# Kernel tuning notes

Measured on AMD Instinct MI355X. Metric: run time of the kernel, lower is better.

The kernel has to match this reference:

```python
import jax, jax.numpy as jnp
import numpy as np

D_MODEL = 1024
NUM_HEADS = 16
SEQ_LEN = 2048
BATCH = 2
THETA = 10000.0


def apply_rope(x, positions, theta=THETA):
    # x: [b, h, s, d]; positions: [s] int
    d = x.shape[-1]
    inv_freq = 1.0 / (theta ** (jnp.arange(0, d, 2, dtype=jnp.float32) / d))  # [d/2]
    ang = positions.astype(jnp.float32)[:, None] * inv_freq[None, :]  # [s, d/2]
    cos, sin = jnp.cos(ang), jnp.sin(ang)  # [s, d/2]
    x_even = x[..., 0::2]
    x_odd = x[..., 1::2]
    out_even = x_even * cos - x_odd * sin
    out_odd = x_even * sin + x_odd * cos
    # re-interleave pairs
    out = jnp.stack([out_even, out_odd], axis=-1).reshape(x.shape)
    return out


def setup_inputs() -> dict:
    key = jax.random.key(0)
    ks = jax.random.split(key, 5)
    scale = 1.0 / np.sqrt(D_MODEL)
    return {
        "in_features": jax.random.normal(ks[0], (BATCH, SEQ_LEN, D_MODEL), dtype=jnp.float32),
        "token_positions": jnp.arange(SEQ_LEN, dtype=jnp.int32),
        "q_w": jax.random.normal(ks[1], (D_MODEL, D_MODEL), dtype=jnp.float32) * scale,
        "k_w": jax.random.normal(ks[2], (D_MODEL, D_MODEL), dtype=jnp.float32) * scale,
        "v_w": jax.random.normal(ks[3], (D_MODEL, D_MODEL), dtype=jnp.float32) * scale,
        "o_w": jax.random.normal(ks[4], (D_MODEL, D_MODEL), dtype=jnp.float32) * scale,
    }


def reference(in_features, token_positions, q_w, k_w, v_w, o_w):
    b, s, _ = in_features.shape
    h = NUM_HEADS
    d_k = D_MODEL // h

    # Linear stores weights [out, in]: y = x @ W^T
    def proj(x, w):
        y = jnp.einsum('bsi,oi->bso', x, w)
        return y.reshape(b, s, h, d_k).transpose(0, 2, 1, 3)  # [b, h, s, d]

    q = apply_rope(proj(in_features, q_w), token_positions)
    k = apply_rope(proj(in_features, k_w), token_positions)
    v = proj(in_features, v_w)

    scores = jnp.einsum('bhqd,bhkd->bhqk', q, k) / jnp.sqrt(jnp.float32(d_k))
    causal = jnp.tril(jnp.ones((s, s), dtype=bool))
    scores = jnp.where(causal, scores, jnp.float32(-1e30))
    attn = jax.nn.softmax(scores, axis=-1)
    out = jnp.einsum('bhqk,bhkd->bhqd', attn, v)  # [b, h, s, d]
    out = out.transpose(0, 2, 1, 3).reshape(b, s, h * d_k)
    return jnp.einsum('bsi,oi->bso', out, o_w)
```

## Files before the change

### kernel.cpp

```cpp
#include <hip/hip_runtime.h>
#include <hip/hip_bf16.h>

typedef unsigned short ushort_t;
typedef unsigned int uint_t;
typedef __attribute__((ext_vector_type(4))) float f32x4;
typedef __attribute__((ext_vector_type(16))) float f32x16;
typedef __attribute__((ext_vector_type(8))) short short8;
typedef __attribute__((ext_vector_type(4))) short short4x;
typedef __attribute__((ext_vector_type(4))) unsigned short u16x4;
typedef __attribute__((ext_vector_type(2))) uint_t u32x2;

typedef const __attribute__((address_space(1))) unsigned char glob_t;
typedef __attribute__((address_space(3))) unsigned char lds_t;

#define S_LEN 2048
#define DM 1024
#define NH 16
#define DH 64
#define NB 2
#define BH (NB*NH)
#define MROWS (NB*S_LEN)

#define SCALE_L2E 0.18033688f

__device__ __forceinline__ float bf2f(ushort_t u) {
    return __uint_as_float(((uint_t)u) << 16);
}
__device__ __forceinline__ ushort_t f2bf(float f) {
    __hip_bfloat16 h = __float2bfloat16(f);
    return *reinterpret_cast<ushort_t*>(&h);
}

__global__ __launch_bounds__(256) void convert_all(
    const float* __restrict__ X,  const float* __restrict__ Wq,
    const float* __restrict__ Wk, const float* __restrict__ Wv,
    const float* __restrict__ Wo,
    ushort_t* __restrict__ Xb,  ushort_t* __restrict__ Wqb,
    ushort_t* __restrict__ Wkb, ushort_t* __restrict__ Wvb,
    ushort_t* __restrict__ Wob)
{
    size_t i = (size_t)blockIdx.x * 256 + threadIdx.x;
    size_t e = i * 4;
    const float* src; ushort_t* dst; size_t off;
    if (e < (size_t)MROWS * DM) { src = X; dst = Xb; off = e; }
    else {
        size_t r = e - (size_t)MROWS * DM;
        int w = (int)(r >> 20); off = r & 1048575;
        src = (w == 0) ? Wq : (w == 1) ? Wk : (w == 2) ? Wv : Wo;
        dst = (w == 0) ? Wqb : (w == 1) ? Wkb : (w == 2) ? Wvb : Wob;
    }
    float4 v = *reinterpret_cast<const float4*>(src + off);
    u16x4 o;
    o[0] = f2bf(v.x); o[1] = f2bf(v.y); o[2] = f2bf(v.z); o[3] = f2bf(v.w);
    *reinterpret_cast<u16x4*>(dst + off) = o;
}

__global__ __launch_bounds__(256) void rope_table_k(
    const int* __restrict__ pos, float2* __restrict__ tab)
{
    int i = blockIdx.x * 256 + threadIdx.x;
    int s = i >> 5, f = i & 31;
    float inv = powf(10000.0f, -(float)f / 32.0f);
    float ang = (float)pos[s] * inv;
    tab[i] = make_float2(cosf(ang), sinf(ang));
}

template<int MODE>
__global__ __launch_bounds__(256) void gemm128b(
    const ushort_t* __restrict__ A,
    const ushort_t* __restrict__ W0, const ushort_t* __restrict__ W1,
    const ushort_t* __restrict__ W2,
    ushort_t* __restrict__ D0, ushort_t* __restrict__ D1,
    ushort_t* __restrict__ D2,
    float* __restrict__ Fout, const float2* __restrict__ tab)
{
    __shared__ __attribute__((aligned(16))) ushort_t As[128 * 32];
    __shared__ __attribute__((aligned(16))) ushort_t Bs[128 * 32];
    const ushort_t* W = (MODE == 1 || blockIdx.z == 0) ? W0
                        : (blockIdx.z == 1 ? W1 : W2);
    ushort_t* Dst = (blockIdx.z == 0) ? D0 : (blockIdx.z == 1) ? D1 : D2;
    int m0 = blockIdx.x * 128, n0 = blockIdx.y * 128;
    int tid = threadIdx.x, lane = tid & 63, wv = tid >> 6;
    int wm = wv >> 1, wn = wv & 1;
    int l15 = lane & 15, g = lane >> 4;

    f32x4 acc[4][4];
    for (int i = 0; i < 4; i++)
        for (int j = 0; j < 4; j++)
            acc[i][j] = (f32x4){0.f, 0.f, 0.f, 0.f};

    int srow = wv * 32 + (lane >> 2);
    int scol = (lane & 3) * 8;
    const ushort_t* Ap = A + (size_t)(m0 + srow) * DM + scol;
    const ushort_t* Wp = W + (size_t)(n0 + srow) * DM + scol;
    lds_t* laA0 = (lds_t*)&As[wv * 1024];
    lds_t* laA1 = (lds_t*)&As[wv * 1024 + 512];
    lds_t* laB0 = (lds_t*)&Bs[wv * 1024];
    lds_t* laB1 = (lds_t*)&Bs[wv * 1024 + 512];

    for (int kk = 0; kk < DM; kk += 32) {
        __builtin_amdgcn_global_load_lds((glob_t*)(Ap + kk), laA0, 16, 0, 0);
        __builtin_amdgcn_global_load_lds((glob_t*)(Ap + 16 * DM + kk), laA1, 16, 0, 0);
        __builtin_amdgcn_global_load_lds((glob_t*)(Wp + kk), laB0, 16, 0, 0);
        __builtin_amdgcn_global_load_lds((glob_t*)(Wp + 16 * DM + kk), laB1, 16, 0, 0);
        __syncthreads();
        short8 af[4], bf[4];
        for (int i = 0; i < 4; i++)
            af[i] = *reinterpret_cast<const short8*>(
                &As[(wm * 64 + i * 16 + l15) * 32 + g * 8]);
        for (int j = 0; j < 4; j++)
            bf[j] = *reinterpret_cast<const short8*>(
                &Bs[(wn * 64 + j * 16 + l15) * 32 + g * 8]);
        __builtin_amdgcn_s_setprio(1);
        for (int i = 0; i < 4; i++)
            for (int j = 0; j < 4; j++)
                acc[i][j] = __builtin_amdgcn_mfma_f32_16x16x32_bf16(
                    af[i], bf[j], acc[i][j], 0, 0, 0);
        __builtin_amdgcn_s_setprio(0);
        __syncthreads();
    }

    for (int i = 0; i < 4; i++) {
        for (int j = 0; j < 4; j++) {
            int mbase = m0 + wm * 64 + i * 16 + g * 4;
            int n = n0 + wn * 64 + j * 16 + l15;
            if (MODE == 0) {
                int h = n >> 6, d = n & 63;
                if (blockIdx.z < 2) {
                    int f = d >> 1;
                    float sgn = (d & 1) ? 1.f : -1.f;
                    float sc = (blockIdx.z == 0) ? SCALE_L2E : 1.0f;
                    for (int r = 0; r < 4; r++) {
                        int m = mbase + r;
                        int b = m >> 11, s = m & 2047;
                        float v = acc[i][j][r];
                        float p = __shfl_xor(v, 1);
                        float2 cs = tab[s * 32 + f];
                        float out = (v * cs.x + p * cs.y * sgn) * sc;
                        Dst[(((size_t)(b * NH + h)) * S_LEN + s) * DH + d] =
                            f2bf(out);
                    }
                } else {
                    for (int r = 0; r < 4; r++) {
                        int m = mbase + r;
                        int b = m >> 11, s = m & 2047;
                        Dst[((size_t)(b * NH + h) * DH + d) * S_LEN + s] =
                            f2bf(acc[i][j][r]);
                    }
                }
            } else {
                for (int r = 0; r < 4; r++)
                    Fout[(size_t)(mbase + r) * DM + n] = acc[i][j][r];
            }
        }
    }
}

#define WAITV4 asm volatile("s_waitcnt vmcnt(4)" ::: "memory")
#define WAITV0 asm volatile("s_waitcnt vmcnt(0)" ::: "memory")

__global__ __launch_bounds__(512, 1) void attn_k10(
    const ushort_t* __restrict__ Q, const ushort_t* __restrict__ K,
    const ushort_t* __restrict__ Vt, ushort_t* __restrict__ O)
{
    __shared__ __attribute__((aligned(16))) ushort_t Ks[3][8192];
    __shared__ __attribute__((aligned(16))) ushort_t Vs[3][8192];

    int tid = threadIdx.x, wv = tid >> 6, lane = tid & 63;
    int l31 = lane & 31, h = lane >> 5, r7 = l31 & 7;
    int bid = blockIdx.x;
    int p = bid >> 5;
    int bh = bid & 31;
    int uB = 15 - p;
    int myu = (wv < 4) ? uB : p;
    int qmin = myu * 128 + (wv & 3) * 32, qmax = qmin + 31;
    int ntr = uB + 1;

    const ushort_t* Qp = Q + (size_t)bh * S_LEN * DH;
    const char* Kp = (const char*)(K + (size_t)bh * S_LEN * DH);
    const char* Vp = (const char*)(Vt + (size_t)bh * DH * S_LEN);

    short8 qf[4];
    {
        const ushort_t* qp = Qp + (((size_t)(qmin + l31)) << 6) + h * 8;
        #pragma unroll
        for (int ds = 0; ds < 4; ds++)
            qf[ds] = *reinterpret_cast<const short8*>(qp + ds * 16);
    }

    f32x16 oacc[2];
    oacc[0] = (f32x16){0.f};
    oacc[1] = (f32x16){0.f};
    float m_run = -INFINITY, l_run = 0.f;

#define STAGE10(buf, kk0) do {                                                \
    _Pragma("unroll") for (int c_ = 0; c_ < 2; ++c_) {                        \
        int Lk_ = c_ * 8192 + tid * 16;                                       \
        int rk_ = Lk_ >> 7;                                                   \
        int ck_ = (Lk_ & 127) ^ ((rk_ & 7) << 4);                             \
        __builtin_amdgcn_global_load_lds(                                     \
            (glob_t*)(Kp + (size_t)((kk0) + rk_) * 128 + ck_),                \
            (lds_t*)((char*)&Ks[buf][0] + c_ * 8192 + wv * 1024), 16, 0, 0);  \
        int rv_ = Lk_ >> 8;                                                   \
        int cb_ = Lk_ & 255;                                                  \
        int cv_ = ((cb_ & 127) ^ ((rv_ & 7) << 4)) | (cb_ & 128);             \
        __builtin_amdgcn_global_load_lds(                                     \
            (glob_t*)(Vp + (size_t)rv_ * (S_LEN * 2) + (size_t)(kk0) * 2      \
                      + cv_),                                                 \
            (lds_t*)((char*)&Vs[buf][0] + c_ * 8192 + wv * 1024), 16, 0, 0);  \
    } } while (0)

    STAGE10(0, 0);
    STAGE10(1, 128);
    WAITV4;
    __builtin_amdgcn_s_barrier();

    int cs = 0;
    for (int t = 0; t < ntr; ++t) {
        int k0 = t << 7;
        int s2 = (cs >= 1) ? cs - 1 : cs + 2;
        bool willstage = (t + 2 < ntr);
        if (willstage) STAGE10(s2, (t + 2) << 7);

        if (k0 <= qmax) {
            const char* kb = (const char*)&Ks[cs][0];
            const char* vbp = (const char*)&Vs[cs][0];

            f32x16 st[4];
            #pragma unroll
            for (int s = 0; s < 4; s++) {
                short8 kf[4];
                #pragma unroll
                for (int ds = 0; ds < 4; ds++)
                    kf[ds] = *reinterpret_cast<const short8*>(
                        kb + (s * 32 + l31) * 128 + (((h + 2 * ds) ^ r7) << 4));
                __builtin_amdgcn_s_setprio(1);
                f32x16 z = {0.f};
                #pragma unroll
                for (int ds = 0; ds < 4; ds++)
                    z = __builtin_amdgcn_mfma_f32_32x32x16_bf16(
                        kf[ds], qf[ds], z, 0, 0, 0);
                st[s] = z;
                __builtin_amdgcn_s_setprio(0);
            }

            if (k0 + 127 > qmin) {
                int q = qmin + l31;
                #pragma unroll
                for (int s = 0; s < 4; s++)
                    #pragma unroll
                    for (int r = 0; r < 16; r++)
                        if ((k0 + s * 32 + (r & 3) + 8 * (r >> 2) + 4 * h) > q)
                            st[s][r] = -1e30f;
            }

            float mv[4];
            #pragma unroll
            for (int s = 0; s < 4; s++) {
                float a0 = fmaxf(st[s][0], st[s][1]);
                float a1 = fmaxf(st[s][2], st[s][3]);
                float a2 = fmaxf(st[s][4], st[s][5]);
                float a3 = fmaxf(st[s][6], st[s][7]);
                float a4 = fmaxf(st[s][8], st[s][9]);
                float a5 = fmaxf(st[s][10], st[s][11]);
                float a6 = fmaxf(st[s][12], st[s][13]);
                float a7 = fmaxf(st[s][14], st[s][15]);
                mv[s] = fmaxf(fmaxf(fmaxf(a0, a1), fmaxf(a2, a3)),
                              fmaxf(fmaxf(a4, a5), fmaxf(a6, a7)));
            }
            float m16 = fmaxf(fmaxf(mv[0], mv[1]), fmaxf(mv[2], mv[3]));
            m16 = fmaxf(m16, __shfl_xor(m16, 32));

            if (!__all(m16 <= m_run + 11.5f)) {
                float m_new = fmaxf(m_run, m16);
                float alpha = exp2f(m_run - m_new);
                m_run = m_new;
                l_run *= alpha;
                oacc[0] *= alpha;
                oacc[1] *= alpha;
            }

            float ps = 0.f;
            short4x pa[4][4];
            #pragma unroll
            for (int s = 0; s < 4; s++)
                #pragma unroll
                for (int kt = 0; kt < 4; kt++) {
                    float p0 = exp2f(st[s][4 * kt + 0] - m_run);
                    float p1 = exp2f(st[s][4 * kt + 1] - m_run);
                    float p2 = exp2f(st[s][4 * kt + 2] - m_run);
                    float p3 = exp2f(st[s][4 * kt + 3] - m_run);
                    ps += (p0 + p1) + (p2 + p3);
                    u32x2 w = { (uint_t)f2bf(p0) | ((uint_t)f2bf(p1) << 16),
                                (uint_t)f2bf(p2) | ((uint_t)f2bf(p3) << 16) };
                    pa[s][kt] = __builtin_bit_cast(short4x, w);
                }
            ps += __shfl_xor(ps, 32);
            l_run += ps;

            #pragma unroll
            for (int s = 0; s < 4; s++) {
                short4x vb[2][4];
                #pragma unroll
                for (int db = 0; db < 2; db++)
                    #pragma unroll
                    for (int kt = 0; kt < 4; kt++) {
                        int c = s * 4 + kt;
                        vb[db][kt] = *reinterpret_cast<const short4x*>(
                            vbp + (db * 32 + l31) * 256
                            + ((((c & 7) ^ r7) << 4) | ((c >> 3) << 7))
                            + h * 8);
                    }
                __builtin_amdgcn_s_setprio(1);
                #pragma unroll
                for (int kt = 0; kt < 4; kt++) {
                    oacc[0] = __builtin_amdgcn_mfma_f32_32x32x8bf16_1k(
                        vb[0][kt], pa[s][kt], oacc[0], 0, 0, 0);
                    oacc[1] = __builtin_amdgcn_mfma_f32_32x32x8bf16_1k(
                        vb[1][kt], pa[s][kt], oacc[1], 0, 0, 0);
                }
                __builtin_amdgcn_s_setprio(0);
            }
        }

        if (willstage) { WAITV4; } else { WAITV0; }
        __builtin_amdgcn_s_barrier();
        cs = (cs >= 2) ? 0 : cs + 1;
    }

    float inv = 1.0f / l_run;
    int b = bh >> 4, head = bh & 15;
    int q_row = qmin + l31;
    size_t obase = ((size_t)b * S_LEN + q_row) * DM + head * DH;
    #pragma unroll
    for (int db = 0; db < 2; db++)
        #pragma unroll
        for (int rg = 0; rg < 4; rg++) {
            u16x4 o;
            #pragma unroll
            for (int j = 0; j < 4; j++)
                o[j] = f2bf(oacc[db][rg * 4 + j] * inv);
            *reinterpret_cast<u16x4*>(&O[obase + db * 32 + rg * 8 + h * 4]) = o;
        }
#undef STAGE10
}

extern "C" void kernel_launch(void* const* d_in, const int* in_sizes, int n_in,
                              void* d_out, int out_size, void* d_ws, size_t ws_size,
                              hipStream_t stream)
{
    const float* X  = (const float*)d_in[0];
    const int* pos  = (const int*)d_in[1];
    const float* qw = (const float*)d_in[2];
    const float* kw = (const float*)d_in[3];
    const float* vw = (const float*)d_in[4];
    const float* ow = (const float*)d_in[5];
    float* out = (float*)d_out;

    char* ws = (char*)d_ws;
    ushort_t* Xb   = (ushort_t*)(ws);
    ushort_t* Wqb  = (ushort_t*)(ws + 8388608);
    ushort_t* Wkb  = (ushort_t*)(ws + 10485760);
    ushort_t* Wvb  = (ushort_t*)(ws + 12582912);
    ushort_t* Wob  = (ushort_t*)(ws + 14680064);
    ushort_t* Qbh  = (ushort_t*)(ws + 16777216);
    ushort_t* Kbh  = (ushort_t*)(ws + 25165824);
    ushort_t* Vtb  = (ushort_t*)(ws + 41943040);
    ushort_t* AttO = (ushort_t*)(ws + 50331648);
    float2*   tab  = (float2*)(ws + 58720256);

    convert_all<<<8192, 256, 0, stream>>>(X, qw, kw, vw, ow,
                                          Xb, Wqb, Wkb, Wvb, Wob);
    rope_table_k<<<256, 256, 0, stream>>>(pos, tab);
    gemm128b<0><<<dim3(32, 8, 3), 256, 0, stream>>>(
        Xb, Wqb, Wkb, Wvb, Qbh, Kbh, Vtb, nullptr, tab);
    attn_k10<<<256, 512, 0, stream>>>(Qbh, Kbh, Vtb, AttO);
    gemm128b<1><<<dim3(32, 8, 1), 256, 0, stream>>>(
        AttO, Wob, nullptr, nullptr, nullptr, nullptr, nullptr, out, tab);
}
```

Before: 132.5 us.

## Merge prep kernels and deepen GEMM K-tile to 64 with XOR-swizzled LDS

Merges the bf16 conversion kernel and the RoPE table kernel into one launch, saving one kernel launch. The projection GEMMs now stage a K-slab of 64 per iteration instead of 32, which halves the number of barrier pairs per tile. They also apply an XOR swizzle on the LDS column offset so that fragment reads avoid bank conflicts. LDS use rises to 32 KB per block, which could reduce occupancy.

```diff
diff --git a/kernel.cpp b/kernel.cpp
--- a/kernel.cpp
+++ b/kernel.cpp
@@ -31,42 +31,41 @@
     return *reinterpret_cast<ushort_t*>(&h);
 }
 
-__global__ __launch_bounds__(256) void convert_all(
+__global__ __launch_bounds__(256) void prep_all(
     const float* __restrict__ X,  const float* __restrict__ Wq,
     const float* __restrict__ Wk, const float* __restrict__ Wv,
-    const float* __restrict__ Wo,
+    const float* __restrict__ Wo, const int* __restrict__ pos,
     ushort_t* __restrict__ Xb,  ushort_t* __restrict__ Wqb,
     ushort_t* __restrict__ Wkb, ushort_t* __restrict__ Wvb,
-    ushort_t* __restrict__ Wob)
+    ushort_t* __restrict__ Wob, float2* __restrict__ tab)
 {
-    size_t i = (size_t)blockIdx.x * 256 + threadIdx.x;
-    size_t e = i * 4;
-    const float* src; ushort_t* dst; size_t off;
-    if (e < (size_t)MROWS * DM) { src = X; dst = Xb; off = e; }
-    else {
-        size_t r = e - (size_t)MROWS * DM;
-        int w = (int)(r >> 20); off = r & 1048575;
-        src = (w == 0) ? Wq : (w == 1) ? Wk : (w == 2) ? Wv : Wo;
-        dst = (w == 0) ? Wqb : (w == 1) ? Wkb : (w == 2) ? Wvb : Wob;
-    }
-    float4 v = *reinterpret_cast<const float4*>(src + off);
-    u16x4 o;
-    o[0] = f2bf(v.x); o[1] = f2bf(v.y); o[2] = f2bf(v.z); o[3] = f2bf(v.w);
-    *reinterpret_cast<u16x4*>(dst + off) = o;
-}
-
-__global__ __launch_bounds__(256) void rope_table_k(
-    const int* __restrict__ pos, float2* __restrict__ tab)
-{
-    int i = blockIdx.x * 256 + threadIdx.x;
-    int s = i >> 5, f = i & 31;
-    float inv = powf(10000.0f, -(float)f / 32.0f);
-    float ang = (float)pos[s] * inv;
-    tab[i] = make_float2(cosf(ang), sinf(ang));
+    int bid = blockIdx.x;
+    if (bid < 8192) {
+        size_t i = (size_t)bid * 256 + threadIdx.x;
+        size_t e = i * 4;
+        const float* src; ushort_t* dst; size_t off;
+        if (e < (size_t)MROWS * DM) { src = X; dst = Xb; off = e; }
+        else {
+            size_t r = e - (size_t)MROWS * DM;
+            int w = (int)(r >> 20); off = r & 1048575;
+            src = (w == 0) ? Wq : (w == 1) ? Wk : (w == 2) ? Wv : Wo;
+            dst = (w == 0) ? Wqb : (w == 1) ? Wkb : (w == 2) ? Wvb : Wob;
+        }
+        float4 v = *reinterpret_cast<const float4*>(src + off);
+        u16x4 o;
+        o[0] = f2bf(v.x); o[1] = f2bf(v.y); o[2] = f2bf(v.z); o[3] = f2bf(v.w);
+        *reinterpret_cast<u16x4*>(dst + off) = o;
+    } else {
+        int i = (bid - 8192) * 256 + threadIdx.x;
+        int s = i >> 5, f = i & 31;
+        float inv = powf(10000.0f, -(float)f / 32.0f);
+        float ang = (float)pos[s] * inv;
+        tab[i] = make_float2(cosf(ang), sinf(ang));
+    }
 }
 
 template<int MODE>
-__global__ __launch_bounds__(256) void gemm128b(
+__global__ __launch_bounds__(256) void gemm128c(
     const ushort_t* __restrict__ A,
     const ushort_t* __restrict__ W0, const ushort_t* __restrict__ W1,
     const ushort_t* __restrict__ W2,
@@ -74,8 +73,8 @@
     ushort_t* __restrict__ D2,
     float* __restrict__ Fout, const float2* __restrict__ tab)
 {
-    __shared__ __attribute__((aligned(16))) ushort_t As[128 * 32];
-    __shared__ __attribute__((aligned(16))) ushort_t Bs[128 * 32];
+    __shared__ __attribute__((aligned(16))) ushort_t As[128 * 64];
+    __shared__ __attribute__((aligned(16))) ushort_t Bs[128 * 64];
     const ushort_t* W = (MODE == 1 || blockIdx.z == 0) ? W0
                         : (blockIdx.z == 1 ? W1 : W2);
     ushort_t* Dst = (blockIdx.z == 0) ? D0 : (blockIdx.z == 1) ? D1 : D2;
@@ -83,40 +82,52 @@
     int tid = threadIdx.x, lane = tid & 63, wv = tid >> 6;
     int wm = wv >> 1, wn = wv & 1;
     int l15 = lane & 15, g = lane >> 4;
+    int r7s = (l15 & 7) << 4;
 
     f32x4 acc[4][4];
     for (int i = 0; i < 4; i++)
         for (int j = 0; j < 4; j++)
             acc[i][j] = (f32x4){0.f, 0.f, 0.f, 0.f};
 
-    int srow = wv * 32 + (lane >> 2);
-    int scol = (lane & 3) * 8;
-    const ushort_t* Ap = A + (size_t)(m0 + srow) * DM + scol;
-    const ushort_t* Wp = W + (size_t)(n0 + srow) * DM + scol;
-    lds_t* laA0 = (lds_t*)&As[wv * 1024];
-    lds_t* laA1 = (lds_t*)&As[wv * 1024 + 512];
-    lds_t* laB0 = (lds_t*)&Bs[wv * 1024];
-    lds_t* laB1 = (lds_t*)&Bs[wv * 1024 + 512];
-
-    for (int kk = 0; kk < DM; kk += 32) {
-        __builtin_amdgcn_global_load_lds((glob_t*)(Ap + kk), laA0, 16, 0, 0);
-        __builtin_amdgcn_global_load_lds((glob_t*)(Ap + 16 * DM + kk), laA1, 16, 0, 0);
-        __builtin_amdgcn_global_load_lds((glob_t*)(Wp + kk), laB0, 16, 0, 0);
-        __builtin_amdgcn_global_load_lds((glob_t*)(Wp + 16 * DM + kk), laB1, 16, 0, 0);
+    const char* Ab = (const char*)A;
+    const char* Wb = (const char*)W;
+
+    for (int kk = 0; kk < DM; kk += 64) {
+        #pragma unroll
+        for (int c = 0; c < 4; c++) {
+            int L = c * 4096 + tid * 16;
+            int row = L >> 7;
+            int colb = (L & 127) ^ ((row & 7) << 4);
+            __builtin_amdgcn_global_load_lds(
+                (glob_t*)(Ab + ((size_t)(m0 + row) * DM + kk) * 2 + colb),
+                (lds_t*)((char*)As + c * 4096 + wv * 1024), 16, 0, 0);
+            __builtin_amdgcn_global_load_lds(
+                (glob_t*)(Wb + ((size_t)(n0 + row) * DM + kk) * 2 + colb),
+                (lds_t*)((char*)Bs + c * 4096 + wv * 1024), 16, 0, 0);
+        }
         __syncthreads();
-        short8 af[4], bf[4];
-        for (int i = 0; i < 4; i++)
-            af[i] = *reinterpret_cast<const short8*>(
-                &As[(wm * 64 + i * 16 + l15) * 32 + g * 8]);
-        for (int j = 0; j < 4; j++)
-            bf[j] = *reinterpret_cast<const short8*>(
-                &Bs[(wn * 64 + j * 16 + l15) * 32 + g * 8]);
-        __builtin_amdgcn_s_setprio(1);
-        for (int i = 0; i < 4; i++)
+        #pragma unroll
+        for (int half = 0; half < 2; half++) {
+            short8 af[4], bf[4];
+            #pragma unroll
+            for (int i = 0; i < 4; i++)
+                af[i] = *reinterpret_cast<const short8*>(
+                    (const char*)As + (wm * 64 + i * 16 + l15) * 128
+                    + ((half * 64 + g * 16) ^ r7s));
+            #pragma unroll
             for (int j = 0; j < 4; j++)
-                acc[i][j] = __builtin_amdgcn_mfma_f32_16x16x32_bf16(
-                    af[i], bf[j], acc[i][j], 0, 0, 0);
-        __builtin_amdgcn_s_setprio(0);
+                bf[j] = *reinterpret_cast<const short8*>(
+                    (const char*)Bs + (wn * 64 + j * 16 + l15) * 128
+                    + ((half * 64 + g * 16) ^ r7s));
+            __builtin_amdgcn_s_setprio(1);
+            #pragma unroll
+            for (int i = 0; i < 4; i++)
+                #pragma unroll
+                for (int j = 0; j < 4; j++)
+                    acc[i][j] = __builtin_amdgcn_mfma_f32_16x16x32_bf16(
+                        af[i], bf[j], acc[i][j], 0, 0, 0);
+            __builtin_amdgcn_s_setprio(0);
+        }
         __syncthreads();
     }
 
@@ -369,12 +380,11 @@
     ushort_t* AttO = (ushort_t*)(ws + 50331648);
     float2*   tab  = (float2*)(ws + 58720256);
 
-    convert_all<<<8192, 256, 0, stream>>>(X, qw, kw, vw, ow,
-                                          Xb, Wqb, Wkb, Wvb, Wob);
-    rope_table_k<<<256, 256, 0, stream>>>(pos, tab);
-    gemm128b<0><<<dim3(32, 8, 3), 256, 0, stream>>>(
+    prep_all<<<8448, 256, 0, stream>>>(X, qw, kw, vw, ow, pos,
+                                       Xb, Wqb, Wkb, Wvb, Wob, tab);
+    gemm128c<0><<<dim3(32, 8, 3), 256, 0, stream>>>(
         Xb, Wqb, Wkb, Wvb, Qbh, Kbh, Vtb, nullptr, tab);
     attn_k10<<<256, 512, 0, stream>>>(Qbh, Kbh, Vtb, AttO);
-    gemm128b<1><<<dim3(32, 8, 1), 256, 0, stream>>>(
+    gemm128c<1><<<dim3(32, 8, 1), 256, 0, stream>>>(
         AttO, Wob, nullptr, nullptr, nullptr, nullptr, nullptr, out, tab);
 }
```

Result: slower. 137.0 us (+3.4%).

## Double-buffer attention K/V in 256-key chunks and merge prep kernels

Applied to the files above, without the earlier changes.

Attention now stages two 128-key tiles per iteration into a double buffer and waits with vmcnt(0) once per 256 keys. Previously it used a 3-deep ring with one barrier per 128 keys. This halves the barrier and loop overhead but reduces how far ahead loads run, and it increases LDS use. The bf16 conversion and RoPE table kernels are fused into one launch to save a kernel launch.

```diff
diff --git a/kernel.cpp b/kernel.cpp
--- a/kernel.cpp
+++ b/kernel.cpp
@@ -31,38 +31,37 @@
     return *reinterpret_cast<ushort_t*>(&h);
 }
 
-__global__ __launch_bounds__(256) void convert_all(
+__global__ __launch_bounds__(256) void prep_all(
     const float* __restrict__ X,  const float* __restrict__ Wq,
     const float* __restrict__ Wk, const float* __restrict__ Wv,
-    const float* __restrict__ Wo,
+    const float* __restrict__ Wo, const int* __restrict__ pos,
     ushort_t* __restrict__ Xb,  ushort_t* __restrict__ Wqb,
     ushort_t* __restrict__ Wkb, ushort_t* __restrict__ Wvb,
-    ushort_t* __restrict__ Wob)
+    ushort_t* __restrict__ Wob, float2* __restrict__ tab)
 {
-    size_t i = (size_t)blockIdx.x * 256 + threadIdx.x;
-    size_t e = i * 4;
-    const float* src; ushort_t* dst; size_t off;
-    if (e < (size_t)MROWS * DM) { src = X; dst = Xb; off = e; }
-    else {
-        size_t r = e - (size_t)MROWS * DM;
-        int w = (int)(r >> 20); off = r & 1048575;
-        src = (w == 0) ? Wq : (w == 1) ? Wk : (w == 2) ? Wv : Wo;
-        dst = (w == 0) ? Wqb : (w == 1) ? Wkb : (w == 2) ? Wvb : Wob;
-    }
-    float4 v = *reinterpret_cast<const float4*>(src + off);
-    u16x4 o;
-    o[0] = f2bf(v.x); o[1] = f2bf(v.y); o[2] = f2bf(v.z); o[3] = f2bf(v.w);
-    *reinterpret_cast<u16x4*>(dst + off) = o;
-}
-
-__global__ __launch_bounds__(256) void rope_table_k(
-    const int* __restrict__ pos, float2* __restrict__ tab)
-{
-    int i = blockIdx.x * 256 + threadIdx.x;
-    int s = i >> 5, f = i & 31;
-    float inv = powf(10000.0f, -(float)f / 32.0f);
-    float ang = (float)pos[s] * inv;
-    tab[i] = make_float2(cosf(ang), sinf(ang));
+    int bid = blockIdx.x;
+    if (bid < 8192) {
+        size_t i = (size_t)bid * 256 + threadIdx.x;
+        size_t e = i * 4;
+        const float* src; ushort_t* dst; size_t off;
+        if (e < (size_t)MROWS * DM) { src = X; dst = Xb; off = e; }
+        else {
+            size_t r = e - (size_t)MROWS * DM;
+            int w = (int)(r >> 20); off = r & 1048575;
+            src = (w == 0) ? Wq : (w == 1) ? Wk : (w == 2) ? Wv : Wo;
+            dst = (w == 0) ? Wqb : (w == 1) ? Wkb : (w == 2) ? Wvb : Wob;
+        }
+        float4 v = *reinterpret_cast<const float4*>(src + off);
+        u16x4 o;
+        o[0] = f2bf(v.x); o[1] = f2bf(v.y); o[2] = f2bf(v.z); o[3] = f2bf(v.w);
+        *reinterpret_cast<u16x4*>(dst + off) = o;
+    } else {
+        int i = (bid - 8192) * 256 + threadIdx.x;
+        int s = i >> 5, f = i & 31;
+        float inv = powf(10000.0f, -(float)f / 32.0f);
+        float ang = (float)pos[s] * inv;
+        tab[i] = make_float2(cosf(ang), sinf(ang));
+    }
 }
 
 template<int MODE>
@@ -156,15 +155,14 @@
     }
 }
 
-#define WAITV4 asm volatile("s_waitcnt vmcnt(4)" ::: "memory")
 #define WAITV0 asm volatile("s_waitcnt vmcnt(0)" ::: "memory")
 
-__global__ __launch_bounds__(512, 1) void attn_k10(
+__global__ __launch_bounds__(512, 1) void attn_k11(
     const ushort_t* __restrict__ Q, const ushort_t* __restrict__ K,
     const ushort_t* __restrict__ Vt, ushort_t* __restrict__ O)
 {
-    __shared__ __attribute__((aligned(16))) ushort_t Ks[3][8192];
-    __shared__ __attribute__((aligned(16))) ushort_t Vs[3][8192];
+    __shared__ __attribute__((aligned(16))) ushort_t Ks[2][2][8192];
+    __shared__ __attribute__((aligned(16))) ushort_t Vs[2][2][8192];
 
     int tid = threadIdx.x, wv = tid >> 6, lane = tid & 63;
     int l31 = lane & 31, h = lane >> 5, r7 = l31 & 7;
@@ -174,7 +172,7 @@
     int uB = 15 - p;
     int myu = (wv < 4) ? uB : p;
     int qmin = myu * 128 + (wv & 3) * 32, qmax = qmin + 31;
-    int ntr = uB + 1;
+    int ntr = (uB + 2) >> 1;
 
     const ushort_t* Qp = Q + (size_t)bh * S_LEN * DH;
     const char* Kp = (const char*)(K + (size_t)bh * S_LEN * DH);
@@ -193,139 +191,146 @@
     oacc[1] = (f32x16){0.f};
     float m_run = -INFINITY, l_run = 0.f;
 
-#define STAGE10(buf, kk0) do {                                                \
+#define STAGE13(buf, hf, kk0) do {                                            \
     _Pragma("unroll") for (int c_ = 0; c_ < 2; ++c_) {                        \
         int Lk_ = c_ * 8192 + tid * 16;                                       \
         int rk_ = Lk_ >> 7;                                                   \
         int ck_ = (Lk_ & 127) ^ ((rk_ & 7) << 4);                             \
         __builtin_amdgcn_global_load_lds(                                     \
             (glob_t*)(Kp + (size_t)((kk0) + rk_) * 128 + ck_),                \
-            (lds_t*)((char*)&Ks[buf][0] + c_ * 8192 + wv * 1024), 16, 0, 0);  \
+            (lds_t*)((char*)&Ks[buf][hf][0] + c_ * 8192 + wv * 1024),         \
+            16, 0, 0);                                                        \
         int rv_ = Lk_ >> 8;                                                   \
         int cb_ = Lk_ & 255;                                                  \
         int cv_ = ((cb_ & 127) ^ ((rv_ & 7) << 4)) | (cb_ & 128);             \
         __builtin_amdgcn_global_load_lds(                                     \
             (glob_t*)(Vp + (size_t)rv_ * (S_LEN * 2) + (size_t)(kk0) * 2      \
                       + cv_),                                                 \
-            (lds_t*)((char*)&Vs[buf][0] + c_ * 8192 + wv * 1024), 16, 0, 0);  \
+            (lds_t*)((char*)&Vs[buf][hf][0] + c_ * 8192 + wv * 1024),         \
+            16, 0, 0);                                                        \
     } } while (0)
 
-    STAGE10(0, 0);
-    STAGE10(1, 128);
-    WAITV4;
+    STAGE13(0, 0, 0);
+    STAGE13(0, 1, 128);
+    WAITV0;
     __builtin_amdgcn_s_barrier();
 
-    int cs = 0;
+    int buf = 0;
     for (int t = 0; t < ntr; ++t) {
-        int k0 = t << 7;
-        int s2 = (cs >= 1) ? cs - 1 : cs + 2;
-        bool willstage = (t + 2 < ntr);
-        if (willstage) STAGE10(s2, (t + 2) << 7);
-
-        if (k0 <= qmax) {
-            const char* kb = (const char*)&Ks[cs][0];
-            const char* vbp = (const char*)&Vs[cs][0];
-
-            f32x16 st[4];
-            #pragma unroll
-            for (int s = 0; s < 4; s++) {
-                short8 kf[4];
+        if (t + 1 < ntr) {
+            STAGE13(buf ^ 1, 0, (t + 1) * 256);
+            STAGE13(buf ^ 1, 1, (t + 1) * 256 + 128);
+        }
+
+        #pragma unroll
+        for (int hf = 0; hf < 2; ++hf) {
+            int k0 = t * 256 + hf * 128;
+            if (k0 <= qmax) {
+                const char* kb = (const char*)&Ks[buf][hf][0];
+                const char* vbp = (const char*)&Vs[buf][hf][0];
+
+                f32x16 st[4];
                 #pragma unroll
-                for (int ds = 0; ds < 4; ds++)
-                    kf[ds] = *reinterpret_cast<const short8*>(
-                        kb + (s * 32 + l31) * 128 + (((h + 2 * ds) ^ r7) << 4));
-                __builtin_amdgcn_s_setprio(1);
-                f32x16 z = {0.f};
+                for (int s = 0; s < 4; s++) {
+                    short8 kf[4];
+                    #pragma unroll
+                    for (int ds = 0; ds < 4; ds++)
+                        kf[ds] = *reinterpret_cast<const short8*>(
+                            kb + (s * 32 + l31) * 128
+                            + (((h + 2 * ds) ^ r7) << 4));
+                    __builtin_amdgcn_s_setprio(1);
+                    f32x16 z = {0.f};
+                    #pragma unroll
+                    for (int ds = 0; ds < 4; ds++)
+                        z = __builtin_amdgcn_mfma_f32_32x32x16_bf16(
+                            kf[ds], qf[ds], z, 0, 0, 0);
+                    st[s] = z;
+                    __builtin_amdgcn_s_setprio(0);
+                }
+
+                if (k0 + 127 > qmin) {
+                    int q = qmin + l31;
+                    #pragma unroll
+                    for (int s = 0; s < 4; s++)
+                        #pragma unroll
+                        for (int r = 0; r < 16; r++)
+                            if ((k0 + s * 32 + (r & 3) + 8 * (r >> 2) + 4 * h) > q)
+                                st[s][r] = -1e30f;
+                }
+
+                float mv[4];
                 #pragma unroll
-                for (int ds = 0; ds < 4; ds++)
-                    z = __builtin_amdgcn_mfma_f32_32x32x16_bf16(
-                        kf[ds], qf[ds], z, 0, 0, 0);
-                st[s] = z;
-                __builtin_amdgcn_s_setprio(0);
-            }
-
-            if (k0 + 127 > qmin) {
-                int q = qmin + l31;
+                for (int s = 0; s < 4; s++) {
+                    float a0 = fmaxf(st[s][0], st[s][1]);
+                    float a1 = fmaxf(st[s][2], st[s][3]);
+                    float a2 = fmaxf(st[s][4], st[s][5]);
+                    float a3 = fmaxf(st[s][6], st[s][7]);
+                    float a4 = fmaxf(st[s][8], st[s][9]);
+                    float a5 = fmaxf(st[s][10], st[s][11]);
+                    float a6 = fmaxf(st[s][12], st[s][13]);
+                    float a7 = fmaxf(st[s][14], st[s][15]);
+                    mv[s] = fmaxf(fmaxf(fmaxf(a0, a1), fmaxf(a2, a3)),
+                                  fmaxf(fmaxf(a4, a5), fmaxf(a6, a7)));
+                }
+                float m16 = fmaxf(fmaxf(mv[0], mv[1]), fmaxf(mv[2], mv[3]));
+                m16 = fmaxf(m16, __shfl_xor(m16, 32));
+
+                if (!__all(m16 <= m_run + 11.5f)) {
+                    float m_new = fmaxf(m_run, m16);
+                    float alpha = exp2f(m_run - m_new);
+                    m_run = m_new;
+                    l_run *= alpha;
+                    oacc[0] *= alpha;
+                    oacc[1] *= alpha;
+                }
+
+                float ps = 0.f;
+                short4x pa[4][4];
                 #pragma unroll
                 for (int s = 0; s < 4; s++)
                     #pragma unroll
-                    for (int r = 0; r < 16; r++)
-                        if ((k0 + s * 32 + (r & 3) + 8 * (r >> 2) + 4 * h) > q)
-                            st[s][r] = -1e30f;
+                    for (int kt = 0; kt < 4; kt++) {
+                        float p0 = exp2f(st[s][4 * kt + 0] - m_run);
+                        float p1 = exp2f(st[s][4 * kt + 1] - m_run);
+                        float p2 = exp2f(st[s][4 * kt + 2] - m_run);
+                        float p3 = exp2f(st[s][4 * kt + 3] - m_run);
+                        ps += (p0 + p1) + (p2 + p3);
+                        u32x2 w = { (uint_t)f2bf(p0) | ((uint_t)f2bf(p1) << 16),
+                                    (uint_t)f2bf(p2) | ((uint_t)f2bf(p3) << 16) };
+                        pa[s][kt] = __builtin_bit_cast(short4x, w);
+                    }
+                ps += __shfl_xor(ps, 32);
+                l_run += ps;
+
+                #pragma unroll
+                for (int s = 0; s < 4; s++) {
+                    short4x vb[2][4];
+                    #pragma unroll
+                    for (int db = 0; db < 2; db++)
+                        #pragma unroll
+                        for (int kt = 0; kt < 4; kt++) {
+                            int c = s * 4 + kt;
+                            vb[db][kt] = *reinterpret_cast<const short4x*>(
+                                vbp + (db * 32 + l31) * 256
+                                + ((((c & 7) ^ r7) << 4) | ((c >> 3) << 7))
+                                + h * 8);
+                        }
+                    __builtin_amdgcn_s_setprio(1);
+                    #pragma unroll
+                    for (int kt = 0; kt < 4; kt++) {
+                        oacc[0] = __builtin_amdgcn_mfma_f32_32x32x8bf16_1k(
+                            vb[0][kt], pa[s][kt], oacc[0], 0, 0, 0);
+                        oacc[1] = __builtin_amdgcn_mfma_f32_32x32x8bf16_1k(
+                            vb[1][kt], pa[s][kt], oacc[1], 0, 0, 0);
+                    }
+                    __builtin_amdgcn_s_setprio(0);
+                }
             }
-
-            float mv[4];
-            #pragma unroll
-            for (int s = 0; s < 4; s++) {
-                float a0 = fmaxf(st[s][0], st[s][1]);
-                float a1 = fmaxf(st[s][2], st[s][3]);
-                float a2 = fmaxf(st[s][4], st[s][5]);
-                float a3 = fmaxf(st[s][6], st[s][7]);
-                float a4 = fmaxf(st[s][8], st[s][9]);
-                float a5 = fmaxf(st[s][10], st[s][11]);
-                float a6 = fmaxf(st[s][12], st[s][13]);
-                float a7 = fmaxf(st[s][14], st[s][15]);
-                mv[s] = fmaxf(fmaxf(fmaxf(a0, a1), fmaxf(a2, a3)),
-                              fmaxf(fmaxf(a4, a5), fmaxf(a6, a7)));
-            }
-            float m16 = fmaxf(fmaxf(mv[0], mv[1]), fmaxf(mv[2], mv[3]));
-            m16 = fmaxf(m16, __shfl_xor(m16, 32));
-
-            if (!__all(m16 <= m_run + 11.5f)) {
-                float m_new = fmaxf(m_run, m16);
-                float alpha = exp2f(m_run - m_new);
-                m_run = m_new;
-                l_run *= alpha;
-                oacc[0] *= alpha;
-                oacc[1] *= alpha;
-            }
-
-            float ps = 0.f;
-            short4x pa[4][4];
-            #pragma unroll
-            for (int s = 0; s < 4; s++)
-                #pragma unroll
-                for (int kt = 0; kt < 4; kt++) {
-                    float p0 = exp2f(st[s][4 * kt + 0] - m_run);
-                    float p1 = exp2f(st[s][4 * kt + 1] - m_run);
-                    float p2 = exp2f(st[s][4 * kt + 2] - m_run);
-                    float p3 = exp2f(st[s][4 * kt + 3] - m_run);
-                    ps += (p0 + p1) + (p2 + p3);
-                    u32x2 w = { (uint_t)f2bf(p0) | ((uint_t)f2bf(p1) << 16),
-                                (uint_t)f2bf(p2) | ((uint_t)f2bf(p3) << 16) };
-                    pa[s][kt] = __builtin_bit_cast(short4x, w);
-                }
-            ps += __shfl_xor(ps, 32);
-            l_run += ps;
-
-            #pragma unroll
-            for (int s = 0; s < 4; s++) {
-                short4x vb[2][4];
-                #pragma unroll
-                for (int db = 0; db < 2; db++)
-                    #pragma unroll
-                    for (int kt = 0; kt < 4; kt++) {
-                        int c = s * 4 + kt;
-                        vb[db][kt] = *reinterpret_cast<const short4x*>(
-                            vbp + (db * 32 + l31) * 256
-                            + ((((c & 7) ^ r7) << 4) | ((c >> 3) << 7))
-                            + h * 8);
-                    }
-                __builtin_amdgcn_s_setprio(1);
-                #pragma unroll
-                for (int kt = 0; kt < 4; kt++) {
-                    oacc[0] = __builtin_amdgcn_mfma_f32_32x32x8bf16_1k(
-                        vb[0][kt], pa[s][kt], oacc[0], 0, 0, 0);
-                    oacc[1] = __builtin_amdgcn_mfma_f32_32x32x8bf16_1k(
-                        vb[1][kt], pa[s][kt], oacc[1], 0, 0, 0);
-                }
-                __builtin_amdgcn_s_setprio(0);
-            }
-        }
-
-        if (willstage) { WAITV4; } else { WAITV0; }
+        }
+
+        WAITV0;
         __builtin_amdgcn_s_barrier();
-        cs = (cs >= 2) ? 0 : cs + 1;
+        buf ^= 1;
     }
 
     float inv = 1.0f / l_run;
@@ -342,7 +347,7 @@
                 o[j] = f2bf(oacc[db][rg * 4 + j] * inv);
             *reinterpret_cast<u16x4*>(&O[obase + db * 32 + rg * 8 + h * 4]) = o;
         }
-#undef STAGE10
+#undef STAGE13
 }
 
 extern "C" void kernel_launch(void* const* d_in, const int* in_sizes, int n_in,
@@ -369,12 +374,11 @@
     ushort_t* AttO = (ushort_t*)(ws + 50331648);
     float2*   tab  = (float2*)(ws + 58720256);
 
-    convert_all<<<8192, 256, 0, stream>>>(X, qw, kw, vw, ow,
-                                          Xb, Wqb, Wkb, Wvb, Wob);
-    rope_table_k<<<256, 256, 0, stream>>>(pos, tab);
+    prep_all<<<8448, 256, 0, stream>>>(X, qw, kw, vw, ow, pos,
+                                       Xb, Wqb, Wkb, Wvb, Wob, tab);
     gemm128b<0><<<dim3(32, 8, 3), 256, 0, stream>>>(
         Xb, Wqb, Wkb, Wvb, Qbh, Kbh, Vtb, nullptr, tab);
-    attn_k10<<<256, 512, 0, stream>>>(Qbh, Kbh, Vtb, AttO);
+    attn_k11<<<256, 512, 0, stream>>>(Qbh, Kbh, Vtb, AttO);
     gemm128b<1><<<dim3(32, 8, 1), 256, 0, stream>>>(
         AttO, Wob, nullptr, nullptr, nullptr, nullptr, nullptr, out, tab);
 }
```

Measured after the change: 126.9 us. 1.04x faster.
